# Kernel optimization log

Hardware: AMD Instinct MI355X
Metric: run time of the kernel (lower is better)

The kernel has to match this reference:

```python
import jax, jax.numpy as jnp
import numpy as np

B, N, D = 4, 4096, 1024
DFF = 4 * D
K = 2048  # max(1, int(N * 0.5))


def setup_inputs() -> dict:
    key = jax.random.key(0)
    ks = jax.random.split(key, 4)
    x = jax.random.normal(ks[0], (B, N, D), dtype=jnp.float32)
    gate_w = jax.random.normal(ks[1], (1, D), dtype=jnp.float32) * 0.02
    w1 = jax.random.normal(ks[2], (D, DFF), dtype=jnp.float32) * (1.0 / np.sqrt(D))
    b1 = jnp.zeros((DFF,), dtype=jnp.float32)
    w2 = jax.random.normal(ks[3], (DFF, D), dtype=jnp.float32) * (1.0 / np.sqrt(DFF))
    b2 = jnp.zeros((D,), dtype=jnp.float32)
    return {"x": x, "gate_w": gate_w, "w1": w1, "b1": b1, "w2": w2, "b2": b2, "k": K}


def reference(x, gate_w, w1, b1, w2, b2, k):
    # scores: [B, N] = gate(x).squeeze(-1)
    scores = jnp.einsum("bnd,d->bn", x, gate_w[0])
    _, topk = jax.lax.top_k(scores, k)          # [B, k] token indices
    # gather selected tokens: [B, k, D]
    x_sel = jnp.take_along_axis(x, topk[:, :, None], axis=1)
    # ffn (d -> 4d -> d, GELU) + residual on selected tokens only
    h = jax.nn.gelu(x_sel @ w1 + b1) @ w2 + b2
    x_proc = x_sel + h
    # scatter processed tokens back into a copy of x
    b_idx = jnp.arange(x.shape[0])[:, None]      # [B, 1]
    out = x.at[b_idx, topk].set(x_proc)
    return out
```

## Files before the change

### kernel.cpp

```cpp
#include <hip/hip_runtime.h>
#include <math.h>

#define B_   4
#define N_   4096
#define D_   1024
#define DFF_ 4096
#define K_   2048

typedef __attribute__((ext_vector_type(8))) short short8;
typedef __attribute__((ext_vector_type(4))) float float4v;

__device__ __forceinline__ unsigned short f2bf(float f) {
    unsigned int u = __float_as_uint(f);
    u = (u + 0x7fffu + ((u >> 16) & 1u)) >> 16;
    return (unsigned short)u;
}

__device__ __forceinline__ void gld16(const void* g, void* l) {
    __builtin_amdgcn_global_load_lds((const __attribute__((address_space(1))) void*)g,
                                     (__attribute__((address_space(3))) void*)l, 16, 0, 0);
}

__global__ __launch_bounds__(256) void scores_kernel(const float* __restrict__ x,
                                                     const float* __restrict__ gate_w,
                                                     float* __restrict__ scores,
                                                     int* __restrict__ slot) {
    int wave = (blockIdx.x * blockDim.x + threadIdx.x) >> 6;
    int lane = threadIdx.x & 63;
    if (wave >= B_ * N_) return;
    if (lane == 1) slot[wave] = -1;
    const float4* xr = (const float4*)(x + (size_t)wave * D_);
    const float4* g  = (const float4*)gate_w;
    float acc = 0.f;
    #pragma unroll
    for (int j = 0; j < D_ / 4 / 64; ++j) {
        float4 a = xr[lane + j * 64];
        float4 b = g[lane + j * 64];
        acc += a.x * b.x + a.y * b.y + a.z * b.z + a.w * b.w;
    }
    #pragma unroll
    for (int off = 32; off > 0; off >>= 1) acc += __shfl_down(acc, off, 64);
    if (lane == 0) scores[wave] = acc;
}

__global__ __launch_bounds__(1024) void select_topk_kernel(const float* __restrict__ scores,
                                                           int* __restrict__ topk,
                                                           int* __restrict__ slot) {
    __shared__ unsigned key[N_];
    __shared__ unsigned hist[256];
    __shared__ int sh_bin, sh_rem, sh_ngt;
    __shared__ int wsum[16], woff[16];
    int b = blockIdx.x, tid = threadIdx.x;
    int lane = tid & 63, wid = tid >> 6;

    for (int i = tid; i < N_; i += 1024) {
        unsigned u = __float_as_uint(scores[b * N_ + i]);
        key[i] = (u & 0x80000000u) ? ~u : (u | 0x80000000u);
    }
    if (tid == 0) sh_ngt = 0;
    __syncthreads();

    unsigned prefix = 0, pmask = 0;
    int rem = K_;
    for (int shift = 24; shift >= 0; shift -= 8) {
        if (tid < 256) hist[tid] = 0;
        __syncthreads();
        for (int i = tid; i < N_; i += 1024) {
            unsigned k = key[i];
            if ((k & pmask) == prefix) atomicAdd(&hist[(k >> shift) & 255u], 1u);
        }
        __syncthreads();
        if (tid < 64) {
            unsigned v0 = hist[4 * lane], v1 = hist[4 * lane + 1];
            unsigned v2 = hist[4 * lane + 2], v3 = hist[4 * lane + 3];
            unsigned s3 = v3, s2 = v2 + s3, s1 = v1 + s2, s0 = v0 + s1;
            unsigned t = s0;
            #pragma unroll
            for (int off = 1; off < 64; off <<= 1) {
                unsigned u = __shfl_down(t, off, 64);
                if (lane + off < 64) t += u;
            }
            unsigned above = t - s0;
            unsigned S0 = s0 + above, S1 = s1 + above, S2 = s2 + above, S3 = s3 + above;
            unsigned R = (unsigned)rem;
            if (S0 >= R && S1 < R) { sh_bin = 4 * lane;     sh_rem = rem - (int)S1; }
            if (S1 >= R && S2 < R) { sh_bin = 4 * lane + 1; sh_rem = rem - (int)S2; }
            if (S2 >= R && S3 < R) { sh_bin = 4 * lane + 2; sh_rem = rem - (int)S3; }
            if (S3 >= R && above < R) { sh_bin = 4 * lane + 3; sh_rem = rem - (int)above; }
        }
        __syncthreads();
        prefix |= ((unsigned)sh_bin) << shift;
        pmask  |= 0xffu << shift;
        rem = sh_rem;
    }
    unsigned T = prefix;
    int c_gt = K_ - rem;

    for (int i = tid; i < N_; i += 1024) {
        bool p = key[i] > T;
        unsigned long long m = __ballot(p);
        int cnt = __popcll(m);
        int basepos = 0;
        if (lane == 0 && cnt) basepos = atomicAdd(&sh_ngt, cnt);
        basepos = __shfl(basepos, 0, 64);
        if (p) {
            int pos = basepos + __popcll(m & ((1ULL << lane) - 1ULL));
            topk[b * K_ + pos] = i;
            slot[b * N_ + i] = b * K_ + pos;
        }
    }
    int base = tid * 4, c = 0;
    #pragma unroll
    for (int j = 0; j < 4; ++j) c += (key[base + j] == T);
    int sc = c;
    #pragma unroll
    for (int off = 1; off < 64; off <<= 1) {
        int u = __shfl_up(sc, off, 64);
        if (lane >= off) sc += u;
    }
    if (lane == 63) wsum[wid] = sc;
    __syncthreads();
    if (tid == 0) {
        int run = 0;
        #pragma unroll
        for (int j = 0; j < 16; ++j) { woff[j] = run; run += wsum[j]; }
    }
    __syncthreads();
    int r = woff[wid] + sc - c;
    #pragma unroll
    for (int j = 0; j < 4; ++j) {
        if (key[base + j] == T) {
            if (r < rem) {
                topk[b * K_ + c_gt + r] = base + j;
                slot[b * N_ + base + j] = b * K_ + c_gt + r;
            }
            ++r;
        }
    }
}

__global__ __launch_bounds__(256) void gather_copy_kernel(const float* __restrict__ x,
                                                          const int* __restrict__ slot,
                                                          unsigned short* __restrict__ xsel,
                                                          float* __restrict__ out) {
    int row = blockIdx.x;
    int t = threadIdx.x;
    int s = slot[row];
    float4 v = ((const float4*)(x + (size_t)row * D_))[t];
    if (s >= 0) {
        ushort4 o;
        o.x = f2bf(v.x); o.y = f2bf(v.y); o.z = f2bf(v.z); o.w = f2bf(v.w);
        ((ushort4*)(xsel + (size_t)s * D_))[t] = o;
    } else {
        ((float4*)(out + (size_t)row * D_))[t] = v;
    }
}

__global__ __launch_bounds__(256) void transpose_both_kernel(const float* __restrict__ w1,
                                                             const float* __restrict__ w2,
                                                             unsigned short* __restrict__ w1t,
                                                             unsigned short* __restrict__ w2t) {
    __shared__ float tile[32][33];
    int bid = blockIdx.x;
    const float* src; unsigned short* dst; int R, C, bx, by;
    if (bid < 4096) { src = w1; dst = w1t; R = D_;   C = DFF_; bx = bid & 127;          by = bid >> 7; }
    else            { src = w2; dst = w2t; R = DFF_; C = D_;   bx = (bid - 4096) & 31;  by = (bid - 4096) >> 5; }
    int tx = threadIdx.x & 31, ty = threadIdx.x >> 5;
    int c = bx * 32 + tx, r0 = by * 32;
    #pragma unroll
    for (int j = ty; j < 32; j += 8) tile[j][tx] = src[(size_t)(r0 + j) * C + c];
    __syncthreads();
    int dc = by * 32 + tx, dr0 = bx * 32;
    #pragma unroll
    for (int j = ty; j < 32; j += 8) dst[(size_t)(dr0 + j) * R + dc] = f2bf(tile[tx][j]);
}


__global__ __launch_bounds__(256, 2) void ffn1_k64_kernel(const unsigned short* __restrict__ A,
                                                          const unsigned short* __restrict__ Bt,
                                                          const float* __restrict__ b1,
                                                          unsigned short* __restrict__ h1) {
    constexpr int K  = D_;
    constexpr int NT = K / 64;
    __shared__ __align__(16) unsigned short smem[32768];

    const int t    = threadIdx.x;
    const int lane = t & 63;
    const int wid  = t >> 6;
    const int quad = lane >> 4;
    const int lr   = lane & 15;
    const int wr   = wid >> 1;
    const int wc   = wid & 1;
    const int row0 = blockIdx.x * 128;
    const int col0 = blockIdx.y * 128;

    const char* aS[4]; const char* bS[4]; int oA[4], oB[4];
    #pragma unroll
    for (int j = 0; j < 4; ++j) {
        int s = t + j * 256;
        int r = s >> 3, c = (s & 7) ^ (r & 7);
        aS[j] = (const char*)A  + ((size_t)(row0 + r) * K + (size_t)c * 8) * 2;
        bS[j] = (const char*)Bt + ((size_t)(col0 + r) * K + (size_t)c * 8) * 2;
        oA[j] = s * 8;
        oB[j] = 8192 + s * 8;
    }

    const int rbA = wr * 64 + lr;
    const int aoff0 = (rbA * 8 + (quad       ^ (rbA & 7))) * 8;
    const int aoff1 = (rbA * 8 + ((4 + quad) ^ (rbA & 7))) * 8;
    const int rbB = wc * 64 + lr;
    const int boff0 = 8192 + (rbB * 8 + (quad       ^ (rbB & 7))) * 8;
    const int boff1 = 8192 + (rbB * 8 + ((4 + quad) ^ (rbB & 7))) * 8;

    unsigned short* lds0 = smem;
    unsigned short* lds1 = smem + 16384;

    #pragma unroll
    for (int j = 0; j < 4; ++j) { gld16(aS[j], lds0 + oA[j]); gld16(bS[j], lds0 + oB[j]); }
    #pragma unroll
    for (int j = 0; j < 4; ++j) { aS[j] += 128; bS[j] += 128; }
    asm volatile("s_waitcnt vmcnt(0)" ::: "memory");
    __builtin_amdgcn_s_barrier();

    float4v acc[4][4] = {};

    auto step = [&](const unsigned short* cur, unsigned short* nxt, bool pf) {
        short8 af[4], bq[4];
        #pragma unroll
        for (int mi = 0; mi < 4; ++mi) af[mi] = *(const short8*)(cur + aoff0 + mi * 1024);
        #pragma unroll
        for (int ni = 0; ni < 4; ++ni) bq[ni] = *(const short8*)(cur + boff0 + ni * 1024);
        if (pf) {
            #pragma unroll
            for (int j = 0; j < 4; ++j) { gld16(aS[j], nxt + oA[j]); gld16(bS[j], nxt + oB[j]); }
            #pragma unroll
            for (int j = 0; j < 4; ++j) { aS[j] += 128; bS[j] += 128; }
        }
        __builtin_amdgcn_sched_barrier(0);
        __builtin_amdgcn_s_setprio(1);
        #pragma unroll
        for (int mi = 0; mi < 4; ++mi)
            #pragma unroll
            for (int ni = 0; ni < 4; ++ni)
                acc[mi][ni] = __builtin_amdgcn_mfma_f32_16x16x32_bf16(af[mi], bq[ni], acc[mi][ni], 0, 0, 0);
        __builtin_amdgcn_s_setprio(0);
        #pragma unroll
        for (int mi = 0; mi < 4; ++mi) af[mi] = *(const short8*)(cur + aoff1 + mi * 1024);
        #pragma unroll
        for (int ni = 0; ni < 4; ++ni) bq[ni] = *(const short8*)(cur + boff1 + ni * 1024);
        __builtin_amdgcn_s_setprio(1);
        #pragma unroll
        for (int mi = 0; mi < 4; ++mi)
            #pragma unroll
            for (int ni = 0; ni < 4; ++ni)
                acc[mi][ni] = __builtin_amdgcn_mfma_f32_16x16x32_bf16(af[mi], bq[ni], acc[mi][ni], 0, 0, 0);
        __builtin_amdgcn_s_setprio(0);
        asm volatile("s_waitcnt vmcnt(0)" ::: "memory");
        __builtin_amdgcn_s_barrier();
    };

    for (int kt = 0; kt < NT - 2; kt += 2) { step(lds0, lds1, true); step(lds1, lds0, true); }
    step(lds0, lds1, true);
    step(lds1, lds0, false);

    float bias[4];
    #pragma unroll
    for (int ni = 0; ni < 4; ++ni) bias[ni] = b1[col0 + wc * 64 + ni * 16 + lr];
    unsigned short* ws_ = smem + wid * 1056;
    const int ro = row0 + wr * 64, co = col0 + wc * 64;
    #pragma unroll
    for (int mi = 0; mi < 4; ++mi) {
        #pragma unroll
        for (int ni = 0; ni < 4; ++ni)
            #pragma unroll
            for (int r = 0; r < 4; ++r) {
                float u = acc[mi][ni][r] + bias[ni];
                float tt = 1.5957691216057308f * u * (1.0f + 0.044715f * u * u);
                float g = u / (1.0f + __expf(-tt));
                ws_[(quad * 4 + r) * 66 + ni * 16 + lr] = f2bf(g);
            }
        asm volatile("s_waitcnt lgkmcnt(0)" ::: "memory");
        #pragma unroll
        for (int j = 0; j < 2; ++j) {
            int chk = lane + j * 64;
            int rr = chk >> 3, cc = chk & 7;
            *(short8*)(h1 + (size_t)(ro + mi * 16 + rr) * DFF_ + co + cc * 8) =
                *(const short8*)(ws_ + rr * 66 + cc * 8);
        }
        asm volatile("s_waitcnt lgkmcnt(0)" ::: "memory");
    }
}

__global__ __launch_bounds__(256, 2) void ffn2_k64_kernel(const unsigned short* __restrict__ A,
                                                          const unsigned short* __restrict__ Bt,
                                                          const float* __restrict__ b2,
                                                          const float* __restrict__ x,
                                                          const int* __restrict__ topk,
                                                          float* __restrict__ out) {
    constexpr int K  = DFF_;
    constexpr int NT = K / 64;
    __shared__ __align__(16) unsigned short smem[32768];

    const int t    = threadIdx.x;
    const int lane = t & 63;
    const int wid  = t >> 6;
    const int quad = lane >> 4;
    const int lr   = lane & 15;
    const int wr   = wid >> 1;
    const int wc   = wid & 1;
    const int row0 = blockIdx.x * 128;
    const int col0 = blockIdx.y * 128;

    const char* aS[4]; const char* bS[4]; int oA[4], oB[4];
    #pragma unroll
    for (int j = 0; j < 4; ++j) {
        int s = t + j * 256;
        int r = s >> 3, c = (s & 7) ^ (r & 7);
        aS[j] = (const char*)A  + ((size_t)(row0 + r) * K + (size_t)c * 8) * 2;
        bS[j] = (const char*)Bt + ((size_t)(col0 + r) * K + (size_t)c * 8) * 2;
        oA[j] = s * 8;
        oB[j] = 8192 + s * 8;
    }

    const int rbA = wr * 64 + lr;
    const int aoff0 = (rbA * 8 + (quad       ^ (rbA & 7))) * 8;
    const int aoff1 = (rbA * 8 + ((4 + quad) ^ (rbA & 7))) * 8;
    const int rbB = wc * 64 + lr;
    const int boff0 = 8192 + (rbB * 8 + (quad       ^ (rbB & 7))) * 8;
    const int boff1 = 8192 + (rbB * 8 + ((4 + quad) ^ (rbB & 7))) * 8;

    unsigned short* lds0 = smem;
    unsigned short* lds1 = smem + 16384;

    #pragma unroll
    for (int j = 0; j < 4; ++j) { gld16(aS[j], lds0 + oA[j]); gld16(bS[j], lds0 + oB[j]); }
    #pragma unroll
    for (int j = 0; j < 4; ++j) { aS[j] += 128; bS[j] += 128; }
    asm volatile("s_waitcnt vmcnt(0)" ::: "memory");
    __builtin_amdgcn_s_barrier();

    float4v acc[4][4] = {};

    auto step = [&](const unsigned short* cur, unsigned short* nxt, bool pf) {
        short8 af[4], bq[4];
        #pragma unroll
        for (int mi = 0; mi < 4; ++mi) af[mi] = *(const short8*)(cur + aoff0 + mi * 1024);
        #pragma unroll
        for (int ni = 0; ni < 4; ++ni) bq[ni] = *(const short8*)(cur + boff0 + ni * 1024);
        if (pf) {
            #pragma unroll
            for (int j = 0; j < 4; ++j) { gld16(aS[j], nxt + oA[j]); gld16(bS[j], nxt + oB[j]); }
            #pragma unroll
            for (int j = 0; j < 4; ++j) { aS[j] += 128; bS[j] += 128; }
        }
        __builtin_amdgcn_sched_barrier(0);
        __builtin_amdgcn_s_setprio(1);
        #pragma unroll
        for (int mi = 0; mi < 4; ++mi)
            #pragma unroll
            for (int ni = 0; ni < 4; ++ni)
                acc[mi][ni] = __builtin_amdgcn_mfma_f32_16x16x32_bf16(af[mi], bq[ni], acc[mi][ni], 0, 0, 0);
        __builtin_amdgcn_s_setprio(0);
        #pragma unroll
        for (int mi = 0; mi < 4; ++mi) af[mi] = *(const short8*)(cur + aoff1 + mi * 1024);
        #pragma unroll
        for (int ni = 0; ni < 4; ++ni) bq[ni] = *(const short8*)(cur + boff1 + ni * 1024);
        __builtin_amdgcn_s_setprio(1);
        #pragma unroll
        for (int mi = 0; mi < 4; ++mi)
            #pragma unroll
            for (int ni = 0; ni < 4; ++ni)
                acc[mi][ni] = __builtin_amdgcn_mfma_f32_16x16x32_bf16(af[mi], bq[ni], acc[mi][ni], 0, 0, 0);
        __builtin_amdgcn_s_setprio(0);
        asm volatile("s_waitcnt vmcnt(0)" ::: "memory");
        __builtin_amdgcn_s_barrier();
    };

    for (int kt = 0; kt < NT - 2; kt += 2) { step(lds0, lds1, true); step(lds1, lds0, true); }
    step(lds0, lds1, true);
    step(lds1, lds0, false);

    #pragma unroll
    for (int mi = 0; mi < 4; ++mi) {
        #pragma unroll
        for (int r = 0; r < 4; ++r) {
            int row = row0 + wr * 64 + mi * 16 + quad * 4 + r;
            int gb = row >> 11;
            int tok = topk[row];
            size_t base = ((size_t)(gb * N_ + tok)) * D_;
            #pragma unroll
            for (int ni = 0; ni < 4; ++ni) {
                int col = col0 + wc * 64 + ni * 16 + lr;
                out[base + col] = x[base + col] + acc[mi][ni][r] + b2[col];
            }
        }
    }
}

extern "C" void kernel_launch(void* const* d_in, const int* in_sizes, int n_in,
                              void* d_out, int out_size, void* d_ws, size_t ws_size,
                              hipStream_t stream) {
    const float* x      = (const float*)d_in[0];
    const float* gate_w = (const float*)d_in[1];
    const float* w1     = (const float*)d_in[2];
    const float* b1     = (const float*)d_in[3];
    const float* w2     = (const float*)d_in[4];
    const float* b2     = (const float*)d_in[5];
    float* out = (float*)d_out;

    char* ws = (char*)d_ws;
    float*          scores = (float*)ws;
    int*            topk   = (int*)(ws + (64 << 10));
    int*            slot   = (int*)(ws + (96 << 10));
    unsigned short* xsel   = (unsigned short*)(ws + (160 << 10));
    unsigned short* w1t    = (unsigned short*)(ws + (160 << 10) + (16 << 20));
    unsigned short* w2t    = (unsigned short*)(ws + (160 << 10) + (24 << 20));
    unsigned short* h1     = (unsigned short*)(ws + (160 << 10) + (32 << 20));

    scores_kernel<<<(B_ * N_) / 4, 256, 0, stream>>>(x, gate_w, scores, slot);
    select_topk_kernel<<<B_, 1024, 0, stream>>>(scores, topk, slot);

    transpose_both_kernel<<<8192, 256, 0, stream>>>(w1, w2, w1t, w2t);

    gather_copy_kernel<<<B_ * N_, 256, 0, stream>>>(x, slot, xsel, out);

    ffn1_k64_kernel<<<dim3(64, 32), 256, 0, stream>>>(xsel, w1t, b1, h1);
    ffn2_k64_kernel<<<dim3(64, 8), 256, 0, stream>>>(h1, w2t, b2, x, topk, out);
}
```

Baseline: 317.9 us.

## Use 256x128 tiles with K=32 stages in FFN1 and remap blocks across XCDs

FFN1 now uses 256x128 output tiles with a K-step of 32, so each wave computes 128x64 and does 8x4 MFMAs per fragment load. This raises arithmetic intensity per LDS read and halves the block count, with a new pair-row swizzled LDS layout and less LDS per block. Both FFN GEMMs switch to a 1D grid whose block index is remapped so that consecutive blocks on the same XCD share A/B tiles, improving L2 locality. The costs are more accumulator registers (which may hurt occupancy at 2 blocks per SM) and twice as many barrier-synchronised K iterations.

```diff
diff --git a/kernel.cpp b/kernel.cpp
--- a/kernel.cpp
+++ b/kernel.cpp
@@ -176,13 +176,13 @@
 }
 
 
-__global__ __launch_bounds__(256, 2) void ffn1_k64_kernel(const unsigned short* __restrict__ A,
-                                                          const unsigned short* __restrict__ Bt,
-                                                          const float* __restrict__ b1,
-                                                          unsigned short* __restrict__ h1) {
+__global__ __launch_bounds__(256, 2) void ffn1_w128_kernel(const unsigned short* __restrict__ A,
+                                                           const unsigned short* __restrict__ Bt,
+                                                           const float* __restrict__ b1,
+                                                           unsigned short* __restrict__ h1) {
     constexpr int K  = D_;
-    constexpr int NT = K / 64;
-    __shared__ __align__(16) unsigned short smem[32768];
+    constexpr int NT = K / 32;
+    __shared__ __align__(16) unsigned short smem[24576];
 
     const int t    = threadIdx.x;
     const int lane = t & 63;
@@ -191,66 +191,68 @@
     const int lr   = lane & 15;
     const int wr   = wid >> 1;
     const int wc   = wid & 1;
-    const int row0 = blockIdx.x * 128;
-    const int col0 = blockIdx.y * 128;
-
-    const char* aS[4]; const char* bS[4]; int oA[4], oB[4];
+    const int L    = (blockIdx.x & 7) * 128 + (blockIdx.x >> 3);
+    const int row0 = (L >> 5) * 256;
+    const int col0 = (L & 31) * 128;
+
+    const char* aS[4]; int oA[4];
+    const char* bS[2]; int oB[2];
     #pragma unroll
     for (int j = 0; j < 4; ++j) {
         int s = t + j * 256;
-        int r = s >> 3, c = (s & 7) ^ (r & 7);
-        aS[j] = (const char*)A  + ((size_t)(row0 + r) * K + (size_t)c * 8) * 2;
-        bS[j] = (const char*)Bt + ((size_t)(col0 + r) * K + (size_t)c * 8) * 2;
+        int rp = s >> 3, w = (s & 7) ^ (rp & 7);
+        aS[j] = (const char*)A + ((size_t)(row0 + rp * 2 + (w >> 2)) * K + (size_t)(w & 3) * 8) * 2;
         oA[j] = s * 8;
+    }
+    #pragma unroll
+    for (int j = 0; j < 2; ++j) {
+        int s = t + j * 256;
+        int rp = s >> 3, w = (s & 7) ^ (rp & 7);
+        bS[j] = (const char*)Bt + ((size_t)(col0 + rp * 2 + (w >> 2)) * K + (size_t)(w & 3) * 8) * 2;
         oB[j] = 8192 + s * 8;
     }
 
-    const int rbA = wr * 64 + lr;
-    const int aoff0 = (rbA * 8 + (quad       ^ (rbA & 7))) * 8;
-    const int aoff1 = (rbA * 8 + ((4 + quad) ^ (rbA & 7))) * 8;
-    const int rbB = wc * 64 + lr;
-    const int boff0 = 8192 + (rbB * 8 + (quad       ^ (rbB & 7))) * 8;
-    const int boff1 = 8192 + (rbB * 8 + ((4 + quad) ^ (rbB & 7))) * 8;
+    const int rbA = wr * 128 + lr, rA2 = rbA >> 1;
+    const int aoff = (rA2 * 8 + ((((rbA & 1) << 2) | quad) ^ (rA2 & 7))) * 8;
+    const int rbB = wc * 64 + lr, rB2 = rbB >> 1;
+    const int boff = 8192 + (rB2 * 8 + ((((rbB & 1) << 2) | quad) ^ (rB2 & 7))) * 8;
 
     unsigned short* lds0 = smem;
-    unsigned short* lds1 = smem + 16384;
-
-    #pragma unroll
-    for (int j = 0; j < 4; ++j) { gld16(aS[j], lds0 + oA[j]); gld16(bS[j], lds0 + oB[j]); }
-    #pragma unroll
-    for (int j = 0; j < 4; ++j) { aS[j] += 128; bS[j] += 128; }
+    unsigned short* lds1 = smem + 12288;
+
+    #pragma unroll
+    for (int j = 0; j < 4; ++j) gld16(aS[j], lds0 + oA[j]);
+    #pragma unroll
+    for (int j = 0; j < 2; ++j) gld16(bS[j], lds0 + oB[j]);
+    #pragma unroll
+    for (int j = 0; j < 4; ++j) aS[j] += 64;
+    #pragma unroll
+    for (int j = 0; j < 2; ++j) bS[j] += 64;
     asm volatile("s_waitcnt vmcnt(0)" ::: "memory");
     __builtin_amdgcn_s_barrier();
 
-    float4v acc[4][4] = {};
+    float4v acc[8][4] = {};
 
     auto step = [&](const unsigned short* cur, unsigned short* nxt, bool pf) {
-        short8 af[4], bq[4];
-        #pragma unroll
-        for (int mi = 0; mi < 4; ++mi) af[mi] = *(const short8*)(cur + aoff0 + mi * 1024);
-        #pragma unroll
-        for (int ni = 0; ni < 4; ++ni) bq[ni] = *(const short8*)(cur + boff0 + ni * 1024);
+        short8 af[8], bq[4];
+        #pragma unroll
+        for (int mi = 0; mi < 8; ++mi) af[mi] = *(const short8*)(cur + aoff + mi * 512);
+        #pragma unroll
+        for (int ni = 0; ni < 4; ++ni) bq[ni] = *(const short8*)(cur + boff + ni * 512);
         if (pf) {
             #pragma unroll
-            for (int j = 0; j < 4; ++j) { gld16(aS[j], nxt + oA[j]); gld16(bS[j], nxt + oB[j]); }
-            #pragma unroll
-            for (int j = 0; j < 4; ++j) { aS[j] += 128; bS[j] += 128; }
+            for (int j = 0; j < 4; ++j) gld16(aS[j], nxt + oA[j]);
+            #pragma unroll
+            for (int j = 0; j < 2; ++j) gld16(bS[j], nxt + oB[j]);
+            #pragma unroll
+            for (int j = 0; j < 4; ++j) aS[j] += 64;
+            #pragma unroll
+            for (int j = 0; j < 2; ++j) bS[j] += 64;
         }
         __builtin_amdgcn_sched_barrier(0);
         __builtin_amdgcn_s_setprio(1);
         #pragma unroll
-        for (int mi = 0; mi < 4; ++mi)
-            #pragma unroll
-            for (int ni = 0; ni < 4; ++ni)
-                acc[mi][ni] = __builtin_amdgcn_mfma_f32_16x16x32_bf16(af[mi], bq[ni], acc[mi][ni], 0, 0, 0);
-        __builtin_amdgcn_s_setprio(0);
-        #pragma unroll
-        for (int mi = 0; mi < 4; ++mi) af[mi] = *(const short8*)(cur + aoff1 + mi * 1024);
-        #pragma unroll
-        for (int ni = 0; ni < 4; ++ni) bq[ni] = *(const short8*)(cur + boff1 + ni * 1024);
-        __builtin_amdgcn_s_setprio(1);
-        #pragma unroll
-        for (int mi = 0; mi < 4; ++mi)
+        for (int mi = 0; mi < 8; ++mi)
             #pragma unroll
             for (int ni = 0; ni < 4; ++ni)
                 acc[mi][ni] = __builtin_amdgcn_mfma_f32_16x16x32_bf16(af[mi], bq[ni], acc[mi][ni], 0, 0, 0);
@@ -267,9 +269,10 @@
     #pragma unroll
     for (int ni = 0; ni < 4; ++ni) bias[ni] = b1[col0 + wc * 64 + ni * 16 + lr];
     unsigned short* ws_ = smem + wid * 1056;
-    const int ro = row0 + wr * 64, co = col0 + wc * 64;
-    #pragma unroll
-    for (int mi = 0; mi < 4; ++mi) {
+    const int co = col0 + wc * 64;
+    #pragma unroll
+    for (int mi = 0; mi < 8; ++mi) {
+        const int ro = row0 + wr * 128 + mi * 16;
         #pragma unroll
         for (int ni = 0; ni < 4; ++ni)
             #pragma unroll
@@ -284,7 +287,7 @@
         for (int j = 0; j < 2; ++j) {
             int chk = lane + j * 64;
             int rr = chk >> 3, cc = chk & 7;
-            *(short8*)(h1 + (size_t)(ro + mi * 16 + rr) * DFF_ + co + cc * 8) =
+            *(short8*)(h1 + (size_t)(ro + rr) * DFF_ + co + cc * 8) =
                 *(const short8*)(ws_ + rr * 66 + cc * 8);
         }
         asm volatile("s_waitcnt lgkmcnt(0)" ::: "memory");
@@ -308,8 +311,9 @@
     const int lr   = lane & 15;
     const int wr   = wid >> 1;
     const int wc   = wid & 1;
-    const int row0 = blockIdx.x * 128;
-    const int col0 = blockIdx.y * 128;
+    const int L    = (blockIdx.x & 7) * 64 + (blockIdx.x >> 3);
+    const int row0 = (L & 63) * 128;
+    const int col0 = (L >> 6) * 128;
 
     const char* aS[4]; const char* bS[4]; int oA[4], oB[4];
     #pragma unroll
@@ -424,6 +428,6 @@
 
     gather_copy_kernel<<<B_ * N_, 256, 0, stream>>>(x, slot, xsel, out);
 
-    ffn1_k64_kernel<<<dim3(64, 32), 256, 0, stream>>>(xsel, w1t, b1, h1);
-    ffn2_k64_kernel<<<dim3(64, 8), 256, 0, stream>>>(h1, w2t, b2, x, topk, out);
-}
+    ffn1_w128_kernel<<<1024, 256, 0, stream>>>(xsel, w1t, b1, h1);
+    ffn2_k64_kernel<<<512, 256, 0, stream>>>(h1, w2t, b2, x, topk, out);
+}
```

Measured after the change: 341.6 us. 1.07x slower.
